# Performance work log

Measured on AMD Instinct MI355X. Metric: run time of the kernel, lower is better.

## Reference

```python
import jax, jax.numpy as jnp
import numpy as np

B, L, H, R, T = 2, 128, 768, 4, 3


def setup_inputs() -> dict:
    key = jax.random.key(0)
    ks = jax.random.split(key, 10)
    s = lambda k, shape: jax.random.normal(k, shape, dtype=jnp.float32) * 0.02
    return {
        "hidden_state": jax.random.normal(ks[0], (B, L, H), dtype=jnp.float32),
        "W_src": s(ks[1], (R * H, H)),
        "b_src": s(ks[2], (R * H,)),
        "W_tgt": s(ks[3], (R * H, H)),
        "b_tgt": s(ks[4], (R * H,)),
        "w_out": s(ks[5], (H,)),
        "dense_W": s(ks[6], (T * H, H)),
        "dense_b": s(ks[7], (T * H,)),
        "clf_W": s(ks[8], (1, H)),
        "clf_b": s(ks[9], (1,)),
    }


def reference(hidden_state, W_src, b_src, W_tgt, b_tgt, w_out,
              dense_W, dense_b, clf_W, clf_b):
    b, l, h = hidden_state.shape
    # Biaffine pairwise relation scoring (dropout = identity at eval).
    h_src = (hidden_state @ W_src.T + b_src).reshape(b, l, R, h)  # [B,L,R,H]
    h_tgt = (hidden_state @ W_tgt.T + b_tgt).reshape(b, l, R, h)  # [B,L,R,H]
    # Pairwise broadcast-add -> tanh -> reduce with w_out. [B,L,L,R,H] intermediate.
    pair = jnp.tanh(h_src[:, :, None, :, :] + h_tgt[:, None, :, :, :])
    relation_logits = jnp.einsum('bstrh,h->bstr', pair, w_out)
    relation_logits = jnp.transpose(relation_logits, (0, 3, 1, 2))  # [B,R,L,L]
    # Token binary classification head.
    z = (hidden_state @ dense_W.T + dense_b).reshape(b, l, T, h)   # [B,L,T,H]
    source_mask_logits = jnp.tanh(z) @ clf_W[0] + clf_b[0]          # [B,L,T]
    source_mask_logits = jnp.transpose(source_mask_logits, (0, 2, 1))  # [B,T,L]
    return relation_logits, source_mask_logits, h_src, h_tgt
```

## Files before the change

kernel.cpp:

```cpp
#include <hip/hip_runtime.h>
#include <hip/hip_bf16.h>

#define LL 128
#define HH 768
#define OFF_REL  0
#define OFF_MASK 131072
#define OFF_HSRC 131840
#define OFF_HTGT 918272
#define SCALEC 2.8853900817779268f

typedef __attribute__((ext_vector_type(8))) short short8;
typedef __attribute__((ext_vector_type(4))) float floatx4;

__device__ inline unsigned short f2bf(float f) {
  unsigned u = __float_as_uint(f);
  u += 0x7FFFu + ((u >> 16) & 1u);
  return (unsigned short)(u >> 16);
}
struct us4 { unsigned short x, y, z, w; };

__device__ __forceinline__ void gload16(const void* g, void* l) {
  __builtin_amdgcn_global_load_lds(
      (const __attribute__((address_space(1))) unsigned int*)g,
      (__attribute__((address_space(3))) unsigned int*)l,
      16, 0, 0);
}

__global__ __launch_bounds__(256) void cvt_kernel(
    const float4* __restrict__ hs, const float4* __restrict__ wsrc,
    const float4* __restrict__ wtgt, const float4* __restrict__ wd,
    us4* __restrict__ ab, us4* __restrict__ wb)
{
  const int n0 = 49152;
  const int n1 = n0 + 589824;
  const int n2 = n1 + 589824;
  const int n3 = n2 + 442368;
  int stride = gridDim.x * blockDim.x;
  for (int i = blockIdx.x * blockDim.x + threadIdx.x; i < n3; i += stride) {
    const float4* src; us4* dst;
    if (i < n0)      { src = hs   + i;        dst = ab + i; }
    else if (i < n1) { src = wsrc + (i - n0); dst = wb + (i - n0); }
    else if (i < n2) { src = wtgt + (i - n1); dst = wb + 589824 + (i - n1); }
    else             { src = wd   + (i - n2); dst = wb + 1179648 + (i - n2); }
    float4 v = *src;
    us4 o; o.x = f2bf(v.x); o.y = f2bf(v.y); o.z = f2bf(v.z); o.w = f2bf(v.w);
    *dst = o;
  }
}

__global__ __launch_bounds__(256, 2) void gemm_kernel(
    const unsigned short* __restrict__ Ab, const unsigned short* __restrict__ Wb,
    const float* __restrict__ b_src, const float* __restrict__ b_tgt,
    const float* __restrict__ dense_b,
    float* __restrict__ out, float* __restrict__ z,
    float* __restrict__ Es, float* __restrict__ Et)
{
  __shared__ __align__(1024) char sAB[3][8192];
  int tid = threadIdx.x;
  int wave = tid >> 6, lane = tid & 63;
  int nb = blockIdx.x, rb = blockIdx.y;
  int gcol0 = nb * 64, grow0 = rb * 64;
  int which = (nb < 48) ? 0 : (nb < 96) ? 1 : 2;

  int srow = wave * 16 + (lane >> 2);
  int sslot = (lane & 3) * 8;
  const unsigned short* gA = Ab + (long)(grow0 + srow) * HH + sslot;
  const unsigned short* gB = Wb + (long)(gcol0 + srow) * HH + sslot;

  int lr = lane & 15, lk16 = (lane >> 4) * 16;
  int wm = (wave >> 1) * 32, wn = (wave & 1) * 32;

  floatx4 acc[2][2];
  #pragma unroll
  for (int mi = 0; mi < 2; ++mi)
    #pragma unroll
    for (int ni = 0; ni < 2; ++ni)
      acc[mi][ni] = (floatx4){0.f, 0.f, 0.f, 0.f};

#define STAGE(BUF, KT) do {                                   \
    char* b_ = &sAB[BUF][0];                                  \
    gload16(gA + (KT) * 32, b_ + wave * 1024);                \
    gload16(gB + (KT) * 32, b_ + 4096 + wave * 1024);         \
  } while (0)

  STAGE(0, 0);
  STAGE(1, 1);

  #pragma unroll 6
  for (int kt = 0; kt < 24; ++kt) {
    int buf = kt % 3;
    if (kt <= 21) {
      STAGE((kt + 2) % 3, kt + 2);
      asm volatile("s_waitcnt vmcnt(4)" ::: "memory");
    } else if (kt == 22) {
      asm volatile("s_waitcnt vmcnt(2)" ::: "memory");
    } else {
      asm volatile("s_waitcnt vmcnt(0)" ::: "memory");
    }
    __builtin_amdgcn_sched_barrier(0);
    __builtin_amdgcn_s_barrier();
    __builtin_amdgcn_sched_barrier(0);

    const char* base = &sAB[buf][0];
    short8 a0 = *(const short8*)(base + (wm + lr) * 64 + lk16);
    short8 a1 = *(const short8*)(base + (wm + 16 + lr) * 64 + lk16);
    short8 b0 = *(const short8*)(base + 4096 + (wn + lr) * 64 + lk16);
    short8 b1 = *(const short8*)(base + 4096 + (wn + 16 + lr) * 64 + lk16);
    acc[0][0] = __builtin_amdgcn_mfma_f32_16x16x32_bf16(a0, b0, acc[0][0], 0, 0, 0);
    acc[0][1] = __builtin_amdgcn_mfma_f32_16x16x32_bf16(a0, b1, acc[0][1], 0, 0, 0);
    acc[1][0] = __builtin_amdgcn_mfma_f32_16x16x32_bf16(a1, b0, acc[1][0], 0, 0, 0);
    acc[1][1] = __builtin_amdgcn_mfma_f32_16x16x32_bf16(a1, b1, acc[1][1], 0, 0, 0);

    __builtin_amdgcn_sched_barrier(0);
    __builtin_amdgcn_s_barrier();
  }
#undef STAGE

  int lrow = (lane >> 4) * 4;
  #pragma unroll
  for (int mi = 0; mi < 2; ++mi)
  #pragma unroll
  for (int ni = 0; ni < 2; ++ni) {
    int colg = gcol0 + wn + ni * 16 + lr;
    int row0 = grow0 + wm + mi * 16 + lrow;
    if (which == 0) {
      float bv = b_src[colg];
      #pragma unroll
      for (int r2 = 0; r2 < 4; ++r2) {
        int row = row0 + r2;
        float v = acc[mi][ni][r2] + bv;
        out[OFF_HSRC + row * 3072 + colg] = v;
        Es[row * 3072 + colg] = __builtin_amdgcn_exp2f(SCALEC * v);
      }
    } else if (which == 1) {
      int cc = colg - 3072;
      float bv = b_tgt[cc];
      #pragma unroll
      for (int r2 = 0; r2 < 4; ++r2) {
        int row = row0 + r2;
        float v = acc[mi][ni][r2] + bv;
        out[OFF_HTGT + row * 3072 + cc] = v;
        Et[row * 3072 + cc] = __builtin_amdgcn_exp2f(SCALEC * v);
      }
    } else {
      int cc = colg - 6144;
      float bv = dense_b[cc];
      #pragma unroll
      for (int r2 = 0; r2 < 4; ++r2)
        z[(row0 + r2) * 2304 + cc] = acc[mi][ni][r2] + bv;
    }
  }
}

#define PHC 256
__global__ __launch_bounds__(512) void pair_kernel(
    const float* __restrict__ Es, const float* __restrict__ Et,
    const float* __restrict__ w_out,
    const float* __restrict__ z, const float* __restrict__ clf_W,
    const float* __restrict__ clf_b, float* __restrict__ out)
{
  int tid = threadIdx.x;

  if (blockIdx.z == 8) {
    int blk = blockIdx.y * 8 + blockIdx.x;
    int wave = tid >> 6, lane = tid & 63;
    int slot = blk * 8 + wave;
    for (int o = slot; o < 768; o += 512) {
      int b = o / 384, rem = o - b * 384;
      int t = rem >> 7, lt = rem & 127;
      const float* zr = z + (long)(b * LL + lt) * 2304 + t * HH;
      float acc = 0.f;
      for (int h = lane; h < HH; h += 64) {
        float x = zr[h];
        float th = 1.f - 2.f * __builtin_amdgcn_rcpf(1.f + __builtin_amdgcn_exp2f(SCALEC * x));
        acc = fmaf(clf_W[h], th, acc);
      }
      #pragma unroll
      for (int d = 32; d; d >>= 1) acc += __shfl_down(acc, d);
      if (lane == 0) out[OFF_MASK + o] = acc + clf_b[0];
    }
    return;
  }

  __shared__ float sA[16][PHC + 4];
  __shared__ float sB[16][PHC + 4];
  __shared__ float sRed[2048];
  __shared__ float sWsum;

  int g = tid >> 6, lane = tid & 63;
  int sq = lane >> 3, tq = lane & 7;
  int t0 = blockIdx.x * 16, s0 = blockIdx.y * 16;
  int br = blockIdx.z, bb = br >> 2, r = br & 3;

  if (tid < 64) {
    float wsm = 0.f;
    for (int h = tid; h < HH; h += 64) wsm += w_out[h];
    #pragma unroll
    for (int d = 32; d; d >>= 1) wsm += __shfl_down(wsm, d);
    if (tid == 0) sWsum = wsm;
  }

  float a00 = 0.f, a01 = 0.f, a10 = 0.f, a11 = 0.f;

  for (int c = 0; c < HH; c += PHC) {
    int offu = __builtin_amdgcn_readfirstlane(c + g * 32);
    float4 wv[8];
    #pragma unroll
    for (int q = 0; q < 8; ++q) wv[q] = *(const float4*)(w_out + offu + q * 4);

    __syncthreads();
    #pragma unroll
    for (int j = 0; j < 2; ++j) {
      int idx = tid * 2 + j;
      int row = idx >> 6, col4 = (idx & 63) * 4;
      *(float4*)&sA[row][col4] =
          *(const float4*)(Es + (long)(bb * LL + s0 + row) * 3072 + r * HH + c + col4);
      *(float4*)&sB[row][col4] =
          *(const float4*)(Et + (long)(bb * LL + t0 + row) * 3072 + r * HH + c + col4);
    }
    __syncthreads();

    const float* pA0 = &sA[2 * sq][g * 32];
    const float* pA1 = &sA[2 * sq + 1][g * 32];
    const float* pB0 = &sB[2 * tq][g * 32];
    const float* pB1 = &sB[2 * tq + 1][g * 32];
    #pragma unroll
    for (int hh = 0; hh < 32; hh += 4) {
      float4 e0 = *(const float4*)(pA0 + hh);
      float4 e1 = *(const float4*)(pA1 + hh);
      float4 f0 = *(const float4*)(pB0 + hh);
      float4 f1 = *(const float4*)(pB1 + hh);
      float4 vw = wv[hh >> 2];
      a00 = fmaf(vw.x, __builtin_amdgcn_rcpf(fmaf(e0.x, f0.x, 1.f)), a00);
      a01 = fmaf(vw.x, __builtin_amdgcn_rcpf(fmaf(e0.x, f1.x, 1.f)), a01);
      a10 = fmaf(vw.x, __builtin_amdgcn_rcpf(fmaf(e1.x, f0.x, 1.f)), a10);
      a11 = fmaf(vw.x, __builtin_amdgcn_rcpf(fmaf(e1.x, f1.x, 1.f)), a11);
      a00 = fmaf(vw.y, __builtin_amdgcn_rcpf(fmaf(e0.y, f0.y, 1.f)), a00);
      a01 = fmaf(vw.y, __builtin_amdgcn_rcpf(fmaf(e0.y, f1.y, 1.f)), a01);
      a10 = fmaf(vw.y, __builtin_amdgcn_rcpf(fmaf(e1.y, f0.y, 1.f)), a10);
      a11 = fmaf(vw.y, __builtin_amdgcn_rcpf(fmaf(e1.y, f1.y, 1.f)), a11);
      a00 = fmaf(vw.z, __builtin_amdgcn_rcpf(fmaf(e0.z, f0.z, 1.f)), a00);
      a01 = fmaf(vw.z, __builtin_amdgcn_rcpf(fmaf(e0.z, f1.z, 1.f)), a01);
      a10 = fmaf(vw.z, __builtin_amdgcn_rcpf(fmaf(e1.z, f0.z, 1.f)), a10);
      a11 = fmaf(vw.z, __builtin_amdgcn_rcpf(fmaf(e1.z, f1.z, 1.f)), a11);
      a00 = fmaf(vw.w, __builtin_amdgcn_rcpf(fmaf(e0.w, f0.w, 1.f)), a00);
      a01 = fmaf(vw.w, __builtin_amdgcn_rcpf(fmaf(e0.w, f1.w, 1.f)), a01);
      a10 = fmaf(vw.w, __builtin_amdgcn_rcpf(fmaf(e1.w, f0.w, 1.f)), a10);
      a11 = fmaf(vw.w, __builtin_amdgcn_rcpf(fmaf(e1.w, f1.w, 1.f)), a11);
    }
  }

  sRed[0 * 512 + g * 64 + lane] = a00;
  sRed[1 * 512 + g * 64 + lane] = a01;
  sRed[2 * 512 + g * 64 + lane] = a10;
  sRed[3 * 512 + g * 64 + lane] = a11;
  __syncthreads();
  if (tid < 256) {
    int s = tid >> 4, t = tid & 15;
    int pp = (s >> 1) * 8 + (t >> 1);
    int sl = (s & 1) * 2 + (t & 1);
    float sum = 0.f;
    #pragma unroll
    for (int gg = 0; gg < 8; ++gg) sum += sRed[sl * 512 + gg * 64 + pp];
    out[((long)br * LL + (s0 + s)) * LL + (t0 + t)] = sWsum - 2.f * sum;
  }
}

extern "C" void kernel_launch(void* const* d_in, const int* in_sizes, int n_in,
                              void* d_out, int out_size, void* d_ws, size_t ws_size,
                              hipStream_t stream)
{
  const float* hidden  = (const float*)d_in[0];
  const float* W_src   = (const float*)d_in[1];
  const float* b_src   = (const float*)d_in[2];
  const float* W_tgt   = (const float*)d_in[3];
  const float* b_tgt   = (const float*)d_in[4];
  const float* w_out   = (const float*)d_in[5];
  const float* dense_W = (const float*)d_in[6];
  const float* dense_b = (const float*)d_in[7];
  const float* clf_W   = (const float*)d_in[8];
  const float* clf_b   = (const float*)d_in[9];
  float* out = (float*)d_out;
  char* ws = (char*)d_ws;

  unsigned short* Ab = (unsigned short*)ws;
  unsigned short* Wb = (unsigned short*)(ws + 393216);
  float* z  = (float*)(ws + 13369344);
  float* Es = (float*)(ws + 15728640);
  float* Et = (float*)(ws + 18874368);

  hipLaunchKernelGGL(cvt_kernel, dim3(2048), dim3(256), 0, stream,
      (const float4*)hidden, (const float4*)W_src, (const float4*)W_tgt,
      (const float4*)dense_W, (us4*)Ab, (us4*)Wb);
  hipLaunchKernelGGL(gemm_kernel, dim3(132, 4), dim3(256), 0, stream,
      Ab, Wb, b_src, b_tgt, dense_b, out, z, Es, Et);
  hipLaunchKernelGGL(pair_kernel, dim3(8, 8, 9), dim3(512), 0, stream,
      Es, Et, w_out, z, clf_W, clf_b, out + OFF_REL);
}
```

Measured before the change: 45.78 us.

## Double GEMM K-tile, deepen pipeline to four stages, swizzle LDS layout

The bf16 MFMA GEMM now loads 64-wide K tiles instead of 32, which halves the iteration count and barrier overhead. The pipeline grows from three to four LDS buffers with three tiles in flight. LDS rows use an XOR swizzle on 16-byte chunks to avoid bank conflicts on the 128-byte-row reads. LDS use rises to 64KB per block, which may cut the two-blocks-per-CU occupancy set by the launch bounds.

After: 43.80 us (median of 2 runs). 4.3% less time.

```diff
diff --git a/kernel.cpp b/kernel.cpp
--- a/kernel.cpp
+++ b/kernel.cpp
@@ -55,20 +55,23 @@
     float* __restrict__ out, float* __restrict__ z,
     float* __restrict__ Es, float* __restrict__ Et)
 {
-  __shared__ __align__(1024) char sAB[3][8192];
+  __shared__ __align__(1024) char sAB[4][16384];
   int tid = threadIdx.x;
   int wave = tid >> 6, lane = tid & 63;
   int nb = blockIdx.x, rb = blockIdx.y;
   int gcol0 = nb * 64, grow0 = rb * 64;
   int which = (nb < 48) ? 0 : (nb < 96) ? 1 : 2;
 
-  int srow = wave * 16 + (lane >> 2);
-  int sslot = (lane & 3) * 8;
-  const unsigned short* gA = Ab + (long)(grow0 + srow) * HH + sslot;
-  const unsigned short* gB = Wb + (long)(gcol0 + srow) * HH + sslot;
-
-  int lr = lane & 15, lk16 = (lane >> 4) * 16;
+  int r0 = tid >> 3, c0 = tid & 7;
+  int c0s = c0 ^ (r0 & 7);
+  const unsigned short* gA0 = Ab + (long)(grow0 + r0) * HH + c0s * 8;
+  const unsigned short* gA1 = gA0 + 32 * HH;
+  const unsigned short* gB0 = Wb + (long)(gcol0 + r0) * HH + c0s * 8;
+  const unsigned short* gB1 = gB0 + 32 * HH;
+
+  int lr = lane & 15, hi = lane >> 4;
   int wm = (wave >> 1) * 32, wn = (wave & 1) * 32;
+  int swz = lr & 7;
 
   floatx4 acc[2][2];
   #pragma unroll
@@ -77,23 +80,28 @@
     for (int ni = 0; ni < 2; ++ni)
       acc[mi][ni] = (floatx4){0.f, 0.f, 0.f, 0.f};
 
-#define STAGE(BUF, KT) do {                                   \
-    char* b_ = &sAB[BUF][0];                                  \
-    gload16(gA + (KT) * 32, b_ + wave * 1024);                \
-    gload16(gB + (KT) * 32, b_ + 4096 + wave * 1024);         \
+#define STAGE(BUF, KT) do {                                       \
+    char* b_ = &sAB[BUF][0];                                      \
+    gload16(gA0 + (KT) * 64, b_ + wave * 1024);                   \
+    gload16(gA1 + (KT) * 64, b_ + 4096 + wave * 1024);            \
+    gload16(gB0 + (KT) * 64, b_ + 8192 + wave * 1024);            \
+    gload16(gB1 + (KT) * 64, b_ + 12288 + wave * 1024);           \
   } while (0)
 
   STAGE(0, 0);
   STAGE(1, 1);
-
-  #pragma unroll 6
-  for (int kt = 0; kt < 24; ++kt) {
-    int buf = kt % 3;
-    if (kt <= 21) {
-      STAGE((kt + 2) % 3, kt + 2);
+  STAGE(2, 2);
+
+  #pragma unroll
+  for (int kt = 0; kt < 12; ++kt) {
+    int buf = kt & 3;
+    if (kt <= 8) {
+      STAGE((kt + 3) & 3, kt + 3);
+      asm volatile("s_waitcnt vmcnt(12)" ::: "memory");
+    } else if (kt == 9) {
+      asm volatile("s_waitcnt vmcnt(8)" ::: "memory");
+    } else if (kt == 10) {
       asm volatile("s_waitcnt vmcnt(4)" ::: "memory");
-    } else if (kt == 22) {
-      asm volatile("s_waitcnt vmcnt(2)" ::: "memory");
     } else {
       asm volatile("s_waitcnt vmcnt(0)" ::: "memory");
     }
@@ -101,22 +109,27 @@
     __builtin_amdgcn_s_barrier();
     __builtin_amdgcn_sched_barrier(0);
 
-    const char* base = &sAB[buf][0];
-    short8 a0 = *(const short8*)(base + (wm + lr) * 64 + lk16);
-    short8 a1 = *(const short8*)(base + (wm + 16 + lr) * 64 + lk16);
-    short8 b0 = *(const short8*)(base + 4096 + (wn + lr) * 64 + lk16);
-    short8 b1 = *(const short8*)(base + 4096 + (wn + 16 + lr) * 64 + lk16);
-    acc[0][0] = __builtin_amdgcn_mfma_f32_16x16x32_bf16(a0, b0, acc[0][0], 0, 0, 0);
-    acc[0][1] = __builtin_amdgcn_mfma_f32_16x16x32_bf16(a0, b1, acc[0][1], 0, 0, 0);
-    acc[1][0] = __builtin_amdgcn_mfma_f32_16x16x32_bf16(a1, b0, acc[1][0], 0, 0, 0);
-    acc[1][1] = __builtin_amdgcn_mfma_f32_16x16x32_bf16(a1, b1, acc[1][1], 0, 0, 0);
+    const char* bA = &sAB[buf][0];
+    const char* bB = bA + 8192;
+    #pragma unroll
+    for (int ks = 0; ks < 2; ++ks) {
+      int cs = ((ks * 4 + hi) ^ swz) * 16;
+      short8 a0 = *(const short8*)(bA + (wm + lr) * 128 + cs);
+      short8 a1 = *(const short8*)(bA + (wm + 16 + lr) * 128 + cs);
+      short8 b0 = *(const short8*)(bB + (wn + lr) * 128 + cs);
+      short8 b1 = *(const short8*)(bB + (wn + 16 + lr) * 128 + cs);
+      acc[0][0] = __builtin_amdgcn_mfma_f32_16x16x32_bf16(a0, b0, acc[0][0], 0, 0, 0);
+      acc[0][1] = __builtin_amdgcn_mfma_f32_16x16x32_bf16(a0, b1, acc[0][1], 0, 0, 0);
+      acc[1][0] = __builtin_amdgcn_mfma_f32_16x16x32_bf16(a1, b0, acc[1][0], 0, 0, 0);
+      acc[1][1] = __builtin_amdgcn_mfma_f32_16x16x32_bf16(a1, b1, acc[1][1], 0, 0, 0);
+    }
 
     __builtin_amdgcn_sched_barrier(0);
     __builtin_amdgcn_s_barrier();
   }
 #undef STAGE
 
-  int lrow = (lane >> 4) * 4;
+  int lrow = hi * 4;
   #pragma unroll
   for (int mi = 0; mi < 2; ++mi)
   #pragma unroll
```
